# Kernel optimization log

Measured on AMD Instinct MI355X. Metric: run time of the kernel, lower is better.

Reference implementation:

```python
import jax, jax.numpy as jnp
import numpy as np

B, S, D, H = 2, 2048, 1024, 16
HD = D // H  # head_dim = 64
SCALE = HD ** -0.5


def setup_inputs() -> dict:
    key = jax.random.key(0)
    ks = jax.random.split(key, 10)
    std = D ** -0.5
    return {
        "x": jax.random.normal(ks[0], (B, S, D), jnp.float32),
        "y": jax.random.normal(ks[1], (B, S, D), jnp.float32),
        "Wq": jax.random.normal(ks[2], (D, D), jnp.float32) * std,
        "bq": jnp.zeros((D,), jnp.float32),
        "Wk": jax.random.normal(ks[3], (D, D), jnp.float32) * std,
        "bk": jnp.zeros((D,), jnp.float32),
        "Wv": jax.random.normal(ks[4], (D, D), jnp.float32) * std,
        "bv": jnp.zeros((D,), jnp.float32),
        "Wo": jax.random.normal(ks[5], (D, D), jnp.float32) * std,
        "bo": jnp.zeros((D,), jnp.float32),
    }


def reference(x, y, Wq, bq, Wk, bk, Wv, bv, Wo, bo):
    # Linear projections (torch Linear: x @ W.T + b; here W stored as [in,out])
    q = x @ Wq + bq  # [B,S,D]
    k = y @ Wk + bk
    v = y @ Wv + bv
    # split heads -> [B,H,S,hd]
    q = q.reshape(B, S, H, HD).transpose(0, 2, 1, 3)
    k = k.reshape(B, S, H, HD).transpose(0, 2, 1, 3)
    v = v.reshape(B, S, H, HD).transpose(0, 2, 1, 3)
    scores = jnp.einsum("bhqd,bhkd->bhqk", q, k) * SCALE  # [B,H,S,S]
    causal = jnp.tril(jnp.ones((S, S), dtype=bool))  # keep lower triangle
    scores = jnp.where(causal[None, None], scores, -jnp.inf)
    attn = jax.nn.softmax(scores, axis=-1)
    out = jnp.einsum("bhqk,bhkd->bhqd", attn, v)  # [B,H,S,hd]
    out = out.transpose(0, 2, 1, 3).reshape(B, S, D)
    return out @ Wo + bo
```

## Files before the change

### kernel.cpp

```cpp
#include <hip/hip_runtime.h>
#include <hip/hip_bf16.h>


#define BDIM 2
#define SDIM 2048
#define DDIM 1024
#define HDIM 16
#define HD   64
#define MDIM (BDIM*SDIM)
#define C2 0.18033688011112042f

using short8  = __attribute__((ext_vector_type(8))) short;
using floatx4 = __attribute__((ext_vector_type(4))) float;

static __device__ __forceinline__ unsigned short f2bf(float x) {
    union { float f; unsigned int u; } c; c.f = x;
    unsigned int r = (c.u + 0x7fffu + ((c.u >> 16) & 1u)) >> 16;
    return (unsigned short)r;
}

static __device__ __forceinline__ unsigned int pack2bf(float a, float b) {
    union { float f; unsigned int u; } ua, ub;
    ua.f = a; ub.f = b;
    return __builtin_amdgcn_perm(ub.u + 0x8000u, ua.u + 0x8000u, 0x07060302u);
}

#define GLD16(g, l) __builtin_amdgcn_global_load_lds(                        \
    (const __attribute__((address_space(1))) void*)(g),                      \
    (__attribute__((address_space(3))) void*)(l), 16, 0, 0)

__global__ __launch_bounds__(256) void cast_bf16_kernel(
    const float* __restrict__ X, const float* __restrict__ Y,
    unsigned short* __restrict__ Xo, unsigned short* __restrict__ Yo)
{
    const float* A    = blockIdx.z ? Y : X;
    unsigned short* O = blockIdx.z ? Yo : Xo;
    const int idx = blockIdx.x * 256 + threadIdx.x;
    const float4 a = ((const float4*)A)[idx*2];
    const float4 b = ((const float4*)A)[idx*2 + 1];
    ushort4 lo, hi;
    lo.x = f2bf(a.x); lo.y = f2bf(a.y); lo.z = f2bf(a.z); lo.w = f2bf(a.w);
    hi.x = f2bf(b.x); hi.y = f2bf(b.y); hi.z = f2bf(b.z); hi.w = f2bf(b.w);
    ((ushort4*)O)[idx*2]     = lo;
    ((ushort4*)O)[idx*2 + 1] = hi;
}

__global__ __launch_bounds__(256) void wtrans_kernel(
    const float* __restrict__ W0, const float* __restrict__ W1,
    const float* __restrict__ W2, const float* __restrict__ W3,
    unsigned short* __restrict__ T0, unsigned short* __restrict__ T1,
    unsigned short* __restrict__ T2, unsigned short* __restrict__ T3)
{
    __shared__ float tile[64][68];
    const int z = blockIdx.z;
    const float* W    = (z == 0) ? W0 : (z == 1) ? W1 : (z == 2) ? W2 : W3;
    unsigned short* T = (z == 0) ? T0 : (z == 1) ? T1 : (z == 2) ? T2 : T3;
    const int k0 = blockIdx.x * 64, n0 = blockIdx.y * 64;
    const int t = threadIdx.x;
    #pragma unroll
    for (int i = 0; i < 4; ++i) {
        const int idx = t + i*256;
        const int kr = idx >> 4, c4 = idx & 15;
        float4 v = *(const float4*)&W[(size_t)(k0 + kr) * DDIM + n0 + c4*4];
        tile[kr][c4*4+0] = v.x; tile[kr][c4*4+1] = v.y;
        tile[kr][c4*4+2] = v.z; tile[kr][c4*4+3] = v.w;
    }
    __syncthreads();
    #pragma unroll
    for (int i = 0; i < 4; ++i) {
        const int idx = t + i*256;
        const int nr = idx >> 4, kc = idx & 15;
        ushort4 o;
        o.x = f2bf(tile[kc*4+0][nr]); o.y = f2bf(tile[kc*4+1][nr]);
        o.z = f2bf(tile[kc*4+2][nr]); o.w = f2bf(tile[kc*4+3][nr]);
        *(ushort4*)&T[(size_t)(n0 + nr) * DDIM + k0 + kc*4] = o;
    }
}

__device__ __forceinline__ void gemm128_core(
    const unsigned short* __restrict__ A, const unsigned short* __restrict__ Bt,
    int bm, int bn, unsigned short* As, unsigned short* Bs, floatx4 acc[4][4])
{
    const int t = threadIdx.x;
    const int w = t >> 6, l = t & 63;
    const int quad = l >> 4, col = l & 15;
    const int wr = (w >> 1) * 64, wc = (w & 1) * 64;

    const int c1 = t + 256;
    const int r0 = t >> 2,  o0 = (t & 3) * 8;
    const int r1 = c1 >> 2, o1 = (c1 & 3) * 8;

    const unsigned short* Ar0 = A  + (size_t)(bm + r0) * DDIM + o0;
    const unsigned short* Ar1 = A  + (size_t)(bm + r1) * DDIM + o1;
    const unsigned short* Br0 = Bt + (size_t)(bn + r0) * DDIM + o0;
    const unsigned short* Br1 = Bt + (size_t)(bn + r1) * DDIM + o1;

    for (int kt = 0; kt < DDIM; kt += 32) {
        __syncthreads();
        GLD16(Ar0 + kt, As + t*8);
        GLD16(Ar1 + kt, As + c1*8);
        GLD16(Br0 + kt, Bs + t*8);
        GLD16(Br1 + kt, Bs + c1*8);
        __syncthreads();
        short8 af[4], bfr[4];
        #pragma unroll
        for (int i = 0; i < 4; ++i)
            af[i] = *(const short8*)&As[(wr + i*16 + col)*32 + quad*8];
        #pragma unroll
        for (int j = 0; j < 4; ++j)
            bfr[j] = *(const short8*)&Bs[(wc + j*16 + col)*32 + quad*8];
        #pragma unroll
        for (int i = 0; i < 4; ++i)
            #pragma unroll
            for (int j = 0; j < 4; ++j)
                acc[i][j] = __builtin_amdgcn_mfma_f32_16x16x32_bf16(
                    af[i], bfr[j], acc[i][j], 0, 0, 0);
    }
}

__global__ __launch_bounds__(256) void qkv_gemm_kernel(
    const unsigned short* __restrict__ xbf, const unsigned short* __restrict__ ybf,
    const unsigned short* __restrict__ Wqt, const unsigned short* __restrict__ Wkt,
    const unsigned short* __restrict__ Wvt,
    const float* __restrict__ bq, const float* __restrict__ bk,
    const float* __restrict__ bv,
    unsigned short* __restrict__ Qbf, unsigned short* __restrict__ Kbf,
    unsigned short* __restrict__ vT)
{
    __shared__ __align__(16) unsigned short As[128*32];
    __shared__ __align__(16) unsigned short Bs[128*32];

    const int z = blockIdx.z;
    const unsigned short* A  = (z == 0) ? xbf : ybf;
    const unsigned short* Wt = (z == 0) ? Wqt : (z == 1) ? Wkt : Wvt;
    const float* bp          = (z == 0) ? bq  : (z == 1) ? bk  : bv;

    const int bm = blockIdx.y * 128, bn = blockIdx.x * 128;
    floatx4 acc[4][4] = {};
    gemm128_core(A, Wt, bm, bn, As, Bs, acc);

    const int t = threadIdx.x;
    const int w = t >> 6, l = t & 63;
    const int quad = l >> 4, col = l & 15;
    const int wr = (w >> 1) * 64, wc = (w & 1) * 64;

    #pragma unroll
    for (int j = 0; j < 4; ++j) {
        const int gn = bn + wc + j*16 + col;
        const float bias = bp[gn];
        #pragma unroll
        for (int i = 0; i < 4; ++i) {
            const int gm0 = bm + wr + i*16 + quad*4;
            if (z == 0) {
                #pragma unroll
                for (int r = 0; r < 4; ++r)
                    Qbf[(size_t)(gm0 + r) * DDIM + gn] = f2bf((acc[i][j][r] + bias) * C2);
            } else if (z == 1) {
                #pragma unroll
                for (int r = 0; r < 4; ++r)
                    Kbf[(size_t)(gm0 + r) * DDIM + gn] = f2bf(acc[i][j][r] + bias);
            } else {
                ushort4 o;
                o.x = f2bf(acc[i][j][0] + bias); o.y = f2bf(acc[i][j][1] + bias);
                o.z = f2bf(acc[i][j][2] + bias); o.w = f2bf(acc[i][j][3] + bias);
                *(ushort4*)&vT[((size_t)((gm0 >> 11) * DDIM + gn)) * SDIM + (gm0 & 2047)] = o;
            }
        }
    }
}

__global__ __launch_bounds__(256) void out_gemm_kernel(
    const unsigned short* __restrict__ Obf, const unsigned short* __restrict__ Wot,
    const float* __restrict__ bo, float* __restrict__ out)
{
    __shared__ __align__(16) unsigned short As[128*32];
    __shared__ __align__(16) unsigned short Bs[128*32];

    const int bm = blockIdx.y * 128, bn = blockIdx.x * 128;
    floatx4 acc[4][4] = {};
    gemm128_core(Obf, Wot, bm, bn, As, Bs, acc);

    const int t = threadIdx.x;
    const int w = t >> 6, l = t & 63;
    const int quad = l >> 4, col = l & 15;
    const int wr = (w >> 1) * 64, wc = (w & 1) * 64;

    #pragma unroll
    for (int j = 0; j < 4; ++j) {
        const int gn = bn + wc + j*16 + col;
        const float bias = bo[gn];
        #pragma unroll
        for (int i = 0; i < 4; ++i) {
            const int gm0 = bm + wr + i*16 + quad*4;
            #pragma unroll
            for (int r = 0; r < 4; ++r)
                out[(size_t)(gm0 + r) * DDIM + gn] = acc[i][j][r] + bias;
        }
    }
}

__global__ __launch_bounds__(256) void attn_mfma_kernel(
    const unsigned short* __restrict__ Qbf, const unsigned short* __restrict__ Kbf,
    const unsigned short* __restrict__ vT, unsigned short* __restrict__ Obf)
{
    __shared__ __align__(16) unsigned short KfL[2][512*8];
    __shared__ __align__(16) unsigned short VfL[2][512*8];
    __shared__ __align__(16) unsigned short PfL[8*1024];

    const int t = threadIdx.x;
    const int w = t >> 6, l = t & 63;
    const int quad = l >> 4, col = l & 15;
    const int jt = blockIdx.x;
    const int h  = blockIdx.y, b = blockIdx.z;
    const size_t hoff = (size_t)h * HD;
    const size_t bS = (size_t)b * SDIM;
    const size_t bD = (size_t)b * DDIM;

    const int qt  = (w < 2) ? jt : (31 - jt);
    const int qwb = qt * 64 + (w & 1) * 32;
    const int nk_wave  = qt + 1;
    const int nk_block = 32 - jt;

    const unsigned short* kp[2];
    const unsigned short* vp[2];
    int kdst[2], vdst[2];
    #pragma unroll
    for (int i = 0; i < 2; ++i) {
        const int f = 2*w + i;
        kp[i]   = Kbf + (bS + (f >> 1)*16 + col) * DDIM + hoff + (f & 1)*32 + quad*8;
        vp[i]   = vT  + (bD + hoff + (f >> 1)*16 + col) * SDIM + (f & 1)*32 + quad*8;
        kdst[i] = (f*64 + l)*8;
        vdst[i] = (f*64 + l)*8;
    }

    short8 qf[2][2];
    #pragma unroll
    for (int qs = 0; qs < 2; ++qs)
        #pragma unroll
        for (int kc = 0; kc < 2; ++kc)
            qf[qs][kc] = *(const short8*)
                &Qbf[(bS + qwb + qs*16 + col) * DDIM + hoff + kc*32 + quad*8];

    float lrun[2] = {0.0f, 0.0f};
    floatx4 o[2][4] = {};

    #pragma unroll
    for (int i = 0; i < 2; ++i) {
        GLD16(kp[i], &KfL[0][kdst[i]]);
        GLD16(vp[i], &VfL[0][vdst[i]]);
    }

    #pragma unroll 1
    for (int it = 0; it < nk_block; ++it) {
        const int ktb = it * 64;
        const int cur = it & 1;
        __syncthreads();
        if (it + 1 < nk_block) {
            const int nxt = cur ^ 1;
            const size_t ko = (size_t)(it + 1) * 64 * DDIM;
            const int    vo = (it + 1) * 64;
            #pragma unroll
            for (int i = 0; i < 2; ++i) {
                GLD16(kp[i] + ko, &KfL[nxt][kdst[i]]);
                GLD16(vp[i] + vo, &VfL[nxt][vdst[i]]);
            }
        }
        if (it >= nk_wave) continue;

        const unsigned short* Kb = KfL[cur];
        const unsigned short* Vb = VfL[cur];
        short8 kf[4][2], vfr[4][2];
        #pragma unroll
        for (int kt = 0; kt < 4; ++kt)
            #pragma unroll
            for (int kc = 0; kc < 2; ++kc)
                kf[kt][kc] = *(const short8*)&Kb[((kt*2 + kc)*64 + l)*8];
        #pragma unroll
        for (int n = 0; n < 4; ++n)
            #pragma unroll
            for (int kk = 0; kk < 2; ++kk)
                vfr[n][kk] = *(const short8*)&Vb[((n*2 + kk)*64 + l)*8];

        #pragma unroll
        for (int qs = 0; qs < 2; ++qs) {
            if (ktb > qwb + qs*16 + 15) continue;

            floatx4 sT[4];
            #pragma unroll
            for (int kt = 0; kt < 4; ++kt) {
                floatx4 z = {};
                z = __builtin_amdgcn_mfma_f32_16x16x32_bf16(kf[kt][0], qf[qs][0], z, 0, 0, 0);
                z = __builtin_amdgcn_mfma_f32_16x16x32_bf16(kf[kt][1], qf[qs][1], z, 0, 0, 0);
                sT[kt] = z;
            }

            const int qrow = qwb + qs*16 + col;
            const bool anymask = (ktb + 63 > qwb + qs*16);
            float p[4][4];
            #pragma unroll
            for (int kt = 0; kt < 4; ++kt)
                #pragma unroll
                for (int r = 0; r < 4; ++r) {
                    float xv = sT[kt][r];
                    if (anymask && (ktb + kt*16 + quad*4 + r > qrow))
                        xv = -1e30f;
                    p[kt][r] = exp2f(xv);
                }

            float st[4];
            #pragma unroll
            for (int kt = 0; kt < 4; ++kt)
                st[kt] = (p[kt][0] + p[kt][1]) + (p[kt][2] + p[kt][3]);
            lrun[qs] += (st[0] + st[1]) + (st[2] + st[3]);

            const int pb = (w*2 + qs) * 1024;
            #pragma unroll
            for (int kt = 0; kt < 4; ++kt) {
                uint2 pk;
                pk.x = pack2bf(p[kt][0], p[kt][1]);
                pk.y = pack2bf(p[kt][2], p[kt][3]);
                *(uint2*)&PfL[pb + ((kt*2 + (quad>>1))*16 + col)*8 + (quad&1)*4] = pk;
            }
            const short8 pf0 = *(const short8*)&PfL[pb + ((0*4 + quad)*16 + col)*8];
            const short8 pf1 = *(const short8*)&PfL[pb + ((1*4 + quad)*16 + col)*8];
            #pragma unroll
            for (int n = 0; n < 4; ++n) {
                o[qs][n] = __builtin_amdgcn_mfma_f32_16x16x32_bf16(vfr[n][0], pf0, o[qs][n], 0, 0, 0);
                o[qs][n] = __builtin_amdgcn_mfma_f32_16x16x32_bf16(vfr[n][1], pf1, o[qs][n], 0, 0, 0);
            }
        }
    }

    #pragma unroll
    for (int qs = 0; qs < 2; ++qs) {
        float lt = lrun[qs];
        lt += __shfl_xor(lt, 16);
        lt += __shfl_xor(lt, 32);
        const float inv = 1.0f / lt;
        #pragma unroll
        for (int n = 0; n < 4; ++n) {
            ushort4 pk;
            pk.x = f2bf(o[qs][n][0] * inv); pk.y = f2bf(o[qs][n][1] * inv);
            pk.z = f2bf(o[qs][n][2] * inv); pk.w = f2bf(o[qs][n][3] * inv);
            *(ushort4*)&Obf[(bS + qwb + qs*16 + col) * DDIM + hoff + n*16 + quad*4] = pk;
        }
    }
}

extern "C" void kernel_launch(void* const* d_in, const int* in_sizes, int n_in,
                              void* d_out, int out_size, void* d_ws, size_t ws_size,
                              hipStream_t stream) {
    const float* x  = (const float*)d_in[0];
    const float* y  = (const float*)d_in[1];
    const float* Wq = (const float*)d_in[2];
    const float* bq = (const float*)d_in[3];
    const float* Wk = (const float*)d_in[4];
    const float* bk = (const float*)d_in[5];
    const float* Wv = (const float*)d_in[6];
    const float* bv = (const float*)d_in[7];
    const float* Wo = (const float*)d_in[8];
    const float* bo = (const float*)d_in[9];
    float* out = (float*)d_out;

    const size_t mat  = (size_t)MDIM * DDIM;
    const size_t wmat = (size_t)DDIM * DDIM;
    unsigned short* p = (unsigned short*)d_ws;
    unsigned short* xbf = p;            p += mat;
    unsigned short* ybf = p;            p += mat;
    unsigned short* Wqt = p;            p += wmat;
    unsigned short* Wkt = p;            p += wmat;
    unsigned short* Wvt = p;            p += wmat;
    unsigned short* Wot = p;            p += wmat;
    unsigned short* Qbf = p;            p += mat;
    unsigned short* Kbf = p;            p += mat;
    unsigned short* vT  = p;            p += mat;
    unsigned short* Obf = p;            p += mat;

    hipLaunchKernelGGL(cast_bf16_kernel, dim3(MDIM*DDIM/8/256, 1, 2), dim3(256),
                       0, stream, x, y, xbf, ybf);
    hipLaunchKernelGGL(wtrans_kernel, dim3(16, 16, 4), dim3(256), 0, stream,
                       Wq, Wk, Wv, Wo, Wqt, Wkt, Wvt, Wot);

    hipLaunchKernelGGL(qkv_gemm_kernel, dim3(DDIM/128, MDIM/128, 3), dim3(256),
                       0, stream, xbf, ybf, Wqt, Wkt, Wvt, bq, bk, bv,
                       Qbf, Kbf, vT);

    hipLaunchKernelGGL(attn_mfma_kernel, dim3(16, HDIM, BDIM), dim3(256),
                       0, stream, Qbf, Kbf, vT, Obf);

    hipLaunchKernelGGL(out_gemm_kernel, dim3(DDIM/128, MDIM/128), dim3(256),
                       0, stream, Obf, Wot, bo, out);
}
```

Baseline: 245.7 us.

## Swap MFMA operands for vectorized row-major epilogue stores and narrow output GEMM tile

The MFMA operands are swapped for the Q/K projections and the output GEMM, so each lane holds four consecutive output columns. Those values can then go out as packed 8-byte bf16 stores or 16-byte float4 stores instead of scattered 2-byte/4-byte column stores. Bias is loaded as float4 to match. The output GEMM tile also shrinks to 128x64, which doubles the block count to 512 for better CU occupancy, at the cost of reloading A tiles more often.

```diff
diff --git a/kernel.cpp b/kernel.cpp
--- a/kernel.cpp
+++ b/kernel.cpp
@@ -77,6 +77,7 @@
     }
 }
 
+template <bool SWAP>
 __device__ __forceinline__ void gemm128_core(
     const unsigned short* __restrict__ A, const unsigned short* __restrict__ Bt,
     int bm, int bn, unsigned short* As, unsigned short* Bs, floatx4 acc[4][4])
@@ -113,8 +114,9 @@
         for (int i = 0; i < 4; ++i)
             #pragma unroll
             for (int j = 0; j < 4; ++j)
-                acc[i][j] = __builtin_amdgcn_mfma_f32_16x16x32_bf16(
-                    af[i], bfr[j], acc[i][j], 0, 0, 0);
+                acc[i][j] = SWAP
+                    ? __builtin_amdgcn_mfma_f32_16x16x32_bf16(bfr[j], af[i], acc[i][j], 0, 0, 0)
+                    : __builtin_amdgcn_mfma_f32_16x16x32_bf16(af[i], bfr[j], acc[i][j], 0, 0, 0);
     }
 }
 
@@ -136,34 +138,50 @@
     const float* bp          = (z == 0) ? bq  : (z == 1) ? bk  : bv;
 
     const int bm = blockIdx.y * 128, bn = blockIdx.x * 128;
-    floatx4 acc[4][4] = {};
-    gemm128_core(A, Wt, bm, bn, As, Bs, acc);
-
     const int t = threadIdx.x;
     const int w = t >> 6, l = t & 63;
     const int quad = l >> 4, col = l & 15;
     const int wr = (w >> 1) * 64, wc = (w & 1) * 64;
 
-    #pragma unroll
-    for (int j = 0; j < 4; ++j) {
-        const int gn = bn + wc + j*16 + col;
-        const float bias = bp[gn];
+    floatx4 acc[4][4] = {};
+
+    if (z < 2) {
+        gemm128_core<true>(A, Wt, bm, bn, As, Bs, acc);
+        unsigned short* O = (z == 0) ? Qbf : Kbf;
+        const float sc = (z == 0) ? C2 : 1.0f;
+        float4 bias4[4];
+        #pragma unroll
+        for (int j = 0; j < 4; ++j)
+            bias4[j] = *(const float4*)&bp[bn + wc + j*16 + quad*4];
         #pragma unroll
         for (int i = 0; i < 4; ++i) {
-            const int gm0 = bm + wr + i*16 + quad*4;
-            if (z == 0) {
-                #pragma unroll
-                for (int r = 0; r < 4; ++r)
-                    Qbf[(size_t)(gm0 + r) * DDIM + gn] = f2bf((acc[i][j][r] + bias) * C2);
-            } else if (z == 1) {
-                #pragma unroll
-                for (int r = 0; r < 4; ++r)
-                    Kbf[(size_t)(gm0 + r) * DDIM + gn] = f2bf(acc[i][j][r] + bias);
-            } else {
-                ushort4 o;
-                o.x = f2bf(acc[i][j][0] + bias); o.y = f2bf(acc[i][j][1] + bias);
-                o.z = f2bf(acc[i][j][2] + bias); o.w = f2bf(acc[i][j][3] + bias);
-                *(ushort4*)&vT[((size_t)((gm0 >> 11) * DDIM + gn)) * SDIM + (gm0 & 2047)] = o;
+            const int m = bm + wr + i*16 + col;
+            unsigned short* rowp = O + (size_t)m * DDIM;
+            #pragma unroll
+            for (int j = 0; j < 4; ++j) {
+                const float v0 = (acc[i][j][0] + bias4[j].x) * sc;
+                const float v1 = (acc[i][j][1] + bias4[j].y) * sc;
+                const float v2 = (acc[i][j][2] + bias4[j].z) * sc;
+                const float v3 = (acc[i][j][3] + bias4[j].w) * sc;
+                uint2 pk;
+                pk.x = pack2bf(v0, v1);
+                pk.y = pack2bf(v2, v3);
+                *(uint2*)&rowp[bn + wc + j*16 + quad*4] = pk;
+            }
+        }
+    } else {
+        gemm128_core<false>(A, Wt, bm, bn, As, Bs, acc);
+        #pragma unroll
+        for (int j = 0; j < 4; ++j) {
+            const int gn = bn + wc + j*16 + col;
+            const float bias = bp[gn];
+            #pragma unroll
+            for (int i = 0; i < 4; ++i) {
+                const int gm0 = bm + wr + i*16 + quad*4;
+                uint2 pk;
+                pk.x = pack2bf(acc[i][j][0] + bias, acc[i][j][1] + bias);
+                pk.y = pack2bf(acc[i][j][2] + bias, acc[i][j][3] + bias);
+                *(uint2*)&vT[((size_t)((gm0 >> 11) * DDIM + gn)) * SDIM + (gm0 & 2047)] = pk;
             }
         }
     }
@@ -174,27 +192,58 @@
     const float* __restrict__ bo, float* __restrict__ out)
 {
     __shared__ __align__(16) unsigned short As[128*32];
-    __shared__ __align__(16) unsigned short Bs[128*32];
-
-    const int bm = blockIdx.y * 128, bn = blockIdx.x * 128;
-    floatx4 acc[4][4] = {};
-    gemm128_core(Obf, Wot, bm, bn, As, Bs, acc);
+    __shared__ __align__(16) unsigned short Bs[64*32];
 
     const int t = threadIdx.x;
     const int w = t >> 6, l = t & 63;
     const int quad = l >> 4, col = l & 15;
-    const int wr = (w >> 1) * 64, wc = (w & 1) * 64;
-
-    #pragma unroll
-    for (int j = 0; j < 4; ++j) {
-        const int gn = bn + wc + j*16 + col;
-        const float bias = bo[gn];
-        #pragma unroll
-        for (int i = 0; i < 4; ++i) {
-            const int gm0 = bm + wr + i*16 + quad*4;
-            #pragma unroll
-            for (int r = 0; r < 4; ++r)
-                out[(size_t)(gm0 + r) * DDIM + gn] = acc[i][j][r] + bias;
+    const int bm = blockIdx.y * 128, bn = blockIdx.x * 64;
+    const int wr = (w >> 1) * 64, wc = (w & 1) * 32;
+
+    const int r0 = t >> 2, o0 = (t & 3) * 8;
+    const unsigned short* Ar0 = Obf + (size_t)(bm + r0) * DDIM + o0;
+    const unsigned short* Ar1 = Obf + (size_t)(bm + 64 + r0) * DDIM + o0;
+    const unsigned short* Br  = Wot + (size_t)(bn + r0) * DDIM + o0;
+
+    floatx4 acc[4][2] = {};
+
+    for (int kt = 0; kt < DDIM; kt += 32) {
+        __syncthreads();
+        GLD16(Ar0 + kt, As + t*8);
+        GLD16(Ar1 + kt, As + (t + 256)*8);
+        GLD16(Br  + kt, Bs + t*8);
+        __syncthreads();
+        short8 af[4], bfr[2];
+        #pragma unroll
+        for (int i = 0; i < 4; ++i)
+            af[i] = *(const short8*)&As[(wr + i*16 + col)*32 + quad*8];
+        #pragma unroll
+        for (int j = 0; j < 2; ++j)
+            bfr[j] = *(const short8*)&Bs[(wc + j*16 + col)*32 + quad*8];
+        #pragma unroll
+        for (int i = 0; i < 4; ++i)
+            #pragma unroll
+            for (int j = 0; j < 2; ++j)
+                acc[i][j] = __builtin_amdgcn_mfma_f32_16x16x32_bf16(
+                    bfr[j], af[i], acc[i][j], 0, 0, 0);
+    }
+
+    float4 bias4[2];
+    #pragma unroll
+    for (int j = 0; j < 2; ++j)
+        bias4[j] = *(const float4*)&bo[bn + wc + j*16 + quad*4];
+    #pragma unroll
+    for (int i = 0; i < 4; ++i) {
+        const int m = bm + wr + i*16 + col;
+        float* rowp = out + (size_t)m * DDIM;
+        #pragma unroll
+        for (int j = 0; j < 2; ++j) {
+            float4 o;
+            o.x = acc[i][j][0] + bias4[j].x;
+            o.y = acc[i][j][1] + bias4[j].y;
+            o.z = acc[i][j][2] + bias4[j].z;
+            o.w = acc[i][j][3] + bias4[j].w;
+            *(float4*)&rowp[bn + wc + j*16 + quad*4] = o;
         }
     }
 }
@@ -388,6 +437,6 @@
     hipLaunchKernelGGL(attn_mfma_kernel, dim3(16, HDIM, BDIM), dim3(256),
                        0, stream, Qbf, Kbf, vT, Obf);
 
-    hipLaunchKernelGGL(out_gemm_kernel, dim3(DDIM/128, MDIM/128), dim3(256),
+    hipLaunchKernelGGL(out_gemm_kernel, dim3(DDIM/64, MDIM/128), dim3(256),
                        0, stream, Obf, Wot, bo, out);
 }
```

New measurement: 244.6 us. No clear change (-0.4%).
